# Performance work log

Measured on AMD Instinct MI355X. Metric: run time of the kernel, lower is better.

Reference implementation:

```python
import jax, jax.numpy as jnp
import numpy as np

SIZE = 896
HALF = SIZE // 2
BINS = 256  # 2 ** (16 / 2)


def _scale(idx):
    # map bin index [0, BINS-1] -> [-1, 1]
    return idx.astype(jnp.float32) / ((BINS - 1) / 2.0) - 1.0


def setup_inputs() -> dict:
    key = jax.random.key(0)
    ks = jax.random.split(key, 13)
    B, T = 32, 256
    rn = lambda k, shape, s: jax.random.normal(k, shape, dtype=jnp.float32) * s
    return {
        "conditional": rn(ks[0], (B, T, 3, SIZE), 0.1),
        "hidden_state": rn(ks[1], (B, SIZE), 0.1),
        "gru_input_bias": rn(ks[2], (3 * SIZE,), 0.1),
        "gru_hidden_weight": rn(ks[3], (3 * SIZE, SIZE), 0.05),
        "gru_hidden_bias": rn(ks[4], (3 * SIZE,), 0.1),
        "w_coarse_in": rn(ks[5], (3 * HALF, 2), 0.5),
        "b_coarse_in": rn(ks[6], (3 * HALF,), 0.1),
        "w_fine_in": rn(ks[7], (3 * HALF, 3), 0.5),
        "b_fine_in": rn(ks[8], (3 * HALF,), 0.1),
        "w_bins_coarse": rn(ks[9], (BINS, HALF), 0.05),
        "b_bins_coarse": rn(ks[10], (BINS,), 0.1),
        "w_bins_fine": rn(ks[11], (BINS, HALF), 0.05),
        "b_bins_fine": rn(ks[12], (BINS,), 0.1),
    }


def reference(conditional, hidden_state, gru_input_bias, gru_hidden_weight,
              gru_hidden_bias, w_coarse_in, b_coarse_in, w_fine_in, b_fine_in,
              w_bins_coarse, b_bins_coarse, w_bins_fine, b_bins_fine):
    B = conditional.shape[0]
    # add GRU input biases per gate (r, u, e)
    cond = conditional + gru_input_bias.reshape(3, SIZE)  # [B,T,3,SIZE]
    # split each gate into coarse/fine halves and regroup: [B,T,3*HALF]
    cond_c = jnp.concatenate([cond[:, :, 0, :HALF], cond[:, :, 1, :HALF], cond[:, :, 2, :HALF]], axis=-1)
    cond_f = jnp.concatenate([cond[:, :, 0, HALF:], cond[:, :, 1, HALF:], cond[:, :, 2, HALF:]], axis=-1)
    cond_c = jnp.swapaxes(cond_c, 0, 1)  # [T,B,3*HALF] time-major for scan
    cond_f = jnp.swapaxes(cond_f, 0, 1)

    # initial go-sample: split_signal(0) -> coarse bin 128, fine bin 0
    coarse0 = jnp.full((B, 1), 128.0 / 127.5 - 1.0, dtype=jnp.float32)
    fine0 = jnp.full((B, 1), -1.0, dtype=jnp.float32)
    ch0 = hidden_state[:, :HALF]
    fh0 = hidden_state[:, HALF:]

    def step(carry, x):
        coarse, fine, ch, fh = carry
        xc, xf = x
        hp = jnp.concatenate([ch, fh], axis=1) @ gru_hidden_weight.T + gru_hidden_bias  # [B,3*SIZE]
        hcr, hfr, hcu, hfu, hce, hfe = jnp.split(hp, 6, axis=1)  # each [B,HALF]
        # ---- coarse half-GRU ----
        ci = jnp.concatenate([coarse, fine], axis=1)  # [B,2]
        cp = ci @ w_coarse_in.T + b_coarse_in + xc  # [B,3*HALF]
        ru = jax.nn.sigmoid(cp[:, :SIZE] + jnp.concatenate([hcr, hcu], axis=1))
        r, u = ru[:, :HALF], ru[:, HALF:]
        e = jnp.tanh(r * hce + cp[:, SIZE:])
        ch = u * ch + (1.0 - u) * e
        c_idx = jnp.argmax(ch @ w_bins_coarse.T + b_bins_coarse, axis=1)  # [B]
        coarse = _scale(c_idx)[:, None]
        # ---- fine half-GRU ----
        fi = jnp.concatenate([ci, coarse], axis=1)  # [B,3]
        fp = fi @ w_fine_in.T + b_fine_in + xf
        ru = jax.nn.sigmoid(fp[:, :SIZE] + jnp.concatenate([hfr, hfu], axis=1))
        r, u = ru[:, :HALF], ru[:, HALF:]
        e = jnp.tanh(r * hfe + fp[:, SIZE:])
        fh = u * fh + (1.0 - u) * e
        f_idx = jnp.argmax(fh @ w_bins_fine.T + b_bins_fine, axis=1)
        fine = _scale(f_idx)[:, None]
        return (coarse, fine, ch, fh), (c_idx, f_idx)

    (_, _, ch, fh), (oc, of) = jax.lax.scan(step, (coarse0, fine0, ch0, fh0), (cond_c, cond_f))
    hidden = jnp.concatenate([ch, fh], axis=1)  # [B,SIZE]
    return jnp.swapaxes(oc, 0, 1), jnp.swapaxes(of, 0, 1), hidden
```

## Files before the change

### kernel.cpp

```cpp
#include <hip/hip_runtime.h>

#define NWG  56
#define NBLK 57
#define NTHR 384
#define TT   256
#define SPLITF   2048.0f
#define INVSPLIT 4.8828125e-4f

typedef _Float16 f16;
typedef __attribute__((ext_vector_type(8))) _Float16 f16x8;
typedef __attribute__((ext_vector_type(4))) float f32x4;

__device__ __forceinline__ float sigacc(float x){ return 1.0f/(1.0f + expf(-x)); }

__device__ __forceinline__ unsigned long long amax_key(float v, int bin, unsigned tag){
  unsigned u = __float_as_uint(v);
  u = (u & 0x80000000u) ? ~u : (u | 0x80000000u);
  return ((unsigned long long)u << 32) | ((unsigned long long)(tag & 0xFFFFu) << 8)
       | (unsigned)(255 - bin);
}

__device__ __forceinline__ int grp_base(int g){ return 448 * ((g < 3) ? (2*g) : (2*g - 5)); }

__device__ __forceinline__ void xchg32(unsigned* p, unsigned v){
  __hip_atomic_exchange(p, v, __ATOMIC_RELAXED, __HIP_MEMORY_SCOPE_AGENT);
}
__device__ __forceinline__ void xchg64(unsigned long long* p, unsigned long long v){
  __hip_atomic_exchange(p, v, __ATOMIC_RELAXED, __HIP_MEMORY_SCOPE_AGENT);
}
__device__ __forceinline__ unsigned ldg32(const unsigned* p){
  return __hip_atomic_load(p, __ATOMIC_RELAXED, __HIP_MEMORY_SCOPE_AGENT);
}
__device__ __forceinline__ unsigned long long ldg64(const void* p){
  return __hip_atomic_load((const unsigned long long*)p, __ATOMIC_RELAXED, __HIP_MEMORY_SCOPE_AGENT);
}
__device__ __forceinline__ void drain(){ asm volatile("s_waitcnt vmcnt(0)" ::: "memory"); }
__device__ __forceinline__ int f16bits(f16 h){
  return (int)__builtin_bit_cast(unsigned short, h);
}

__global__ void pack_gru(const float* __restrict__ W, f16* __restrict__ outH, f16* __restrict__ outL){
  int blk = blockIdx.x;
  int ks  = blk % 14;
  int rest= blk / 14;
  int wv  = rest % 6, w = rest / 6;
  int mt  = wv >> 1, kh = wv & 1;
  int l   = threadIdx.x;
  int lr  = mt*16 + (l & 15);
  int R   = grp_base(lr >> 3) + 8*w + (lr & 7);
  int k   = kh*448 + ks*32 + (l >> 4)*8;
  const float* src = W + (size_t)R*896 + k;
  f16x8 vh, vl;
  #pragma unroll
  for (int i=0;i<8;i++){
    float x = src[i];
    f16 h = (f16)x;
    vh[i] = h;
    vl[i] = (f16)((x - (float)h) * SPLITF);
  }
  size_t o = (size_t)blk*64 + l;
  ((f16x8*)outH)[o] = vh;
  ((f16x8*)outL)[o] = vl;
}

__global__ void pack_bins(const float* __restrict__ Wc, const float* __restrict__ Wf,
                          f16* __restrict__ oCh, f16* __restrict__ oCl,
                          f16* __restrict__ oFh, f16* __restrict__ oFl){
  int blk  = blockIdx.x;
  int half = blk / 224;
  int rem  = blk % 224;
  int ks   = rem % 14, wg = rem / 14;
  int l    = threadIdx.x;
  const float* W = half ? Wf : Wc;
  f16* oh = half ? oFh : oCh;
  f16* ol = half ? oFl : oCl;
  int bin = wg*16 + (l & 15);
  int k   = ks*32 + (l >> 4)*8;
  const float* src = W + (size_t)bin*448 + k;
  f16x8 vh, vl;
  #pragma unroll
  for (int i=0;i<8;i++){
    float x = src[i];
    f16 h = (f16)x;
    vh[i] = h;
    vl[i] = (f16)((x - (float)h) * SPLITF);
  }
  size_t o = (size_t)rem*64 + l;
  ((f16x8*)oh)[o] = vh;
  ((f16x8*)ol)[o] = vl;
}

__launch_bounds__(NTHR, 1)
__global__ void wavernn_main(
    const float* __restrict__ cond,
    const float* __restrict__ h0,
    const float* __restrict__ gib,
    const float* __restrict__ ghb,
    const float* __restrict__ wci,
    const float* __restrict__ bci,
    const float* __restrict__ wfi,
    const float* __restrict__ bfi,
    const float* __restrict__ bbc,
    const float* __restrict__ bbf,
    const f16*  __restrict__ wsAh, const f16* __restrict__ wsAl,
    const f16*  __restrict__ wsBCh, const f16* __restrict__ wsBCl,
    const f16*  __restrict__ wsBFh, const f16* __restrict__ wsBFl,
    unsigned*   __restrict__ Hg,
    unsigned long long* __restrict__ partC,
    unsigned long long* __restrict__ partF,
    unsigned*   __restrict__ flags,
    unsigned*   __restrict__ resC,
    unsigned*   __restrict__ resF,
    float* __restrict__ out)
{
  __shared__ float hpL[48][33];
  __shared__ float coarseL[32], fineL[32];
  __shared__ f16x8 binBh0[896], binBl0[896], binBh1[896], binBl1[896];
  __shared__ float wclL[3][8][2], bclL[3][8], wflL[3][8][3], bflL[3][8], hblL[48];

  const int w   = blockIdx.x;
  const int tid = threadIdx.x;
  const int wv  = tid >> 6;
  const int l   = tid & 63;

  auto poll_parts = [&](const unsigned long long* part, unsigned tgt)->unsigned long long {
    int bb = l & 31;
    unsigned long long k0,k1,k2,k3,k4,k5,k6,k7,k8,k9,k10,k11,k12,k13,k14,k15;
    for(;;){
      k0=ldg64(&part[0*32+bb]);  k1=ldg64(&part[1*32+bb]);
      k2=ldg64(&part[2*32+bb]);  k3=ldg64(&part[3*32+bb]);
      k4=ldg64(&part[4*32+bb]);  k5=ldg64(&part[5*32+bb]);
      k6=ldg64(&part[6*32+bb]);  k7=ldg64(&part[7*32+bb]);
      k8=ldg64(&part[8*32+bb]);  k9=ldg64(&part[9*32+bb]);
      k10=ldg64(&part[10*32+bb]); k11=ldg64(&part[11*32+bb]);
      k12=ldg64(&part[12*32+bb]); k13=ldg64(&part[13*32+bb]);
      k14=ldg64(&part[14*32+bb]); k15=ldg64(&part[15*32+bb]);
      unsigned long long tmask = 0xFFFF00ull, texp = (unsigned long long)tgt << 8;
      bool ok = ((k0&tmask)==texp) & ((k1&tmask)==texp) & ((k2&tmask)==texp) & ((k3&tmask)==texp)
              & ((k4&tmask)==texp) & ((k5&tmask)==texp) & ((k6&tmask)==texp) & ((k7&tmask)==texp)
              & ((k8&tmask)==texp) & ((k9&tmask)==texp) & ((k10&tmask)==texp)& ((k11&tmask)==texp)
              & ((k12&tmask)==texp)& ((k13&tmask)==texp)& ((k14&tmask)==texp)& ((k15&tmask)==texp);
      if (__all(ok)) break;
      __builtin_amdgcn_s_sleep(1);
    }
    unsigned long long m01=k0>k1?k0:k1, m23=k2>k3?k2:k3, m45=k4>k5?k4:k5, m67=k6>k7?k6:k7;
    unsigned long long m89=k8>k9?k8:k9, mab=k10>k11?k10:k11, mcd=k12>k13?k12:k13, mef=k14>k15?k14:k15;
    unsigned long long a=m01>m23?m01:m23, c2=m45>m67?m45:m67, d=m89>mab?m89:mab, f=mcd>mef?mcd:mef;
    unsigned long long x=a>c2?a:c2, y=d>f?d:f;
    return x>y?x:y;
  };

  if (w == NWG) {
    if (wv == 0) {
      for (int t=0; t<TT; t++){
        unsigned tgt = (unsigned)(t+1);
        unsigned long long best = poll_parts(partC, tgt);
        int bin = 255 - (int)(best & 0xFFull);
        if (l < 32) {
          out[l*TT + t] = (float)bin;
          xchg32(&resC[l], (tgt << 16) | (unsigned)bin);
        }
      }
    } else if (wv == 1) {
      for (int t=0; t<TT; t++){
        unsigned tgt = (unsigned)(t+1);
        unsigned long long best = poll_parts(partF, tgt);
        int bin = 255 - (int)(best & 0xFFull);
        if (l < 32) {
          out[8192 + l*TT + t] = (float)bin;
          xchg32(&resF[l], (tgt << 16) | (unsigned)bin);
        }
      }
    }
    return;
  }

  const int b   = tid >> 3, e = tid & 7;
  const bool owner = tid < 256;
  const int jc  = 8*w + e;

  unsigned* fE0 = flags;
  unsigned* fE1 = flags + 64;
  unsigned* fE3 = flags + 128;

  const int g_kh = (wv >= 2 && wv <= 4) ? 0 : 1;
  const int g_mt = (wv >= 2 && wv <= 4) ? (wv - 2) : (wv == 5 ? 2 : wv);

  f16x8 afh[14], afl[14];
  {
    const f16x8* Ah = (const f16x8*)wsAh + (size_t)(w*6 + (g_mt*2 + g_kh))*14*64;
    const f16x8* Al = (const f16x8*)wsAl + (size_t)(w*6 + (g_mt*2 + g_kh))*14*64;
    #pragma unroll
    for (int ks=0; ks<14; ks++){ afh[ks] = Ah[ks*64 + l]; afl[ks] = Al[ks*64 + l]; }
  }
  if (w < 16) {
    const f16x8* s0 = (const f16x8*)wsBCh + (size_t)w*896;
    const f16x8* s1 = (const f16x8*)wsBCl + (size_t)w*896;
    const f16x8* s2 = (const f16x8*)wsBFh + (size_t)w*896;
    const f16x8* s3 = (const f16x8*)wsBFl + (size_t)w*896;
    for (int i = tid; i < 896; i += NTHR) {
      binBh0[i] = s0[i]; binBl0[i] = s1[i];
      binBh1[i] = s2[i]; binBl1[i] = s3[i];
    }
  }
  if (tid < 48) hblL[tid] = ghb[grp_base(tid>>3) + 8*w + (tid&7)];
  if (tid < 24) {
    int p = tid >> 3, ee = tid & 7;
    int j = p*448 + 8*w + ee;
    wclL[p][ee][0] = wci[j*2+0]; wclL[p][ee][1] = wci[j*2+1];
    bclL[p][ee]    = bci[j] + gib[p*896 + 8*w + ee];
    wflL[p][ee][0] = wfi[j*3+0]; wflL[p][ee][1] = wfi[j*3+1]; wflL[p][ee][2] = wfi[j*3+2];
    bflL[p][ee]    = bfi[j] + gib[p*896 + 448 + 8*w + ee];
  }
  if (tid < 32) { coarseL[tid] = 128.0f/127.5f - 1.0f; fineL[tid] = -1.0f; }
  float biasC = 0.f, biasF = 0.f;
  if (w < 16) { biasC = bbc[w*16 + (l&15)]; biasF = bbf[w*16 + (l&15)]; }

  auto store_half = [&](unsigned* Hrow, int fine, float val){
    f16 hh = (f16)val;
    f16 hl = (f16)((val - (float)hh) * SPLITF);
    int pk = f16bits(hh) | (f16bits(hl) << 16);
    int nb = __shfl_down(pk, 1);
    if (!(e & 1)) {
      int off = fine*224 + (jc >> 1);
      unsigned hi32 = (unsigned)((pk & 0xffff) | (nb << 16));
      unsigned lo32 = ((unsigned)pk >> 16) | ((unsigned)nb & 0xffff0000u);
      xchg32(Hrow + off,       hi32);
      xchg32(Hrow + 448 + off, lo32);
    }
  };

  auto wait56 = [&](const unsigned* f, int n, unsigned tgt){
    const unsigned* p = f + ((l < n) ? l : 0);
    for(;;){
      unsigned v = ldg32(p);
      if (__all(v == tgt)) break;
      __builtin_amdgcn_s_sleep(1);
    }
    unsigned vv = __hip_atomic_load(p, __ATOMIC_ACQUIRE, __HIP_MEMORY_SCOPE_AGENT);
    asm volatile("" :: "v"(vv) : "memory");
  };
  auto poll_res = [&](const unsigned* res, unsigned tgt)->int{
    const unsigned* p = res + (l & 31);
    unsigned v;
    for(;;){
      v = ldg32(p);
      if (__all((v >> 16) == tgt)) break;
      __builtin_amdgcn_s_sleep(1);
    }
    asm volatile("" ::: "memory");
    return (int)(v & 0xFFFFu);
  };

  float chS = 0.f, fhS = 0.f;
  if (owner) {
    chS = h0[b*896 + jc];
    fhS = h0[b*896 + 448 + jc];
    unsigned* Hrow = Hg + b*896;
    store_half(Hrow, 0, chS);
    store_half(Hrow, 1, fhS);
  }
  drain();
  __syncthreads();
  if (tid == 0) xchg32(&fE0[w], 1u);
  if (wv == 0) wait56(fE0, 56, 1u);
  __syncthreads();

  float xcr=0, xcu=0, xce=0, xfr=0, xfu=0, xfe=0;
  auto prefetch = [&](int t){
    if (owner) {
      const float* cb_ = cond + ((size_t)b*TT + t)*2688;
      xcr = cb_[jc];        xcu = cb_[896 + jc];  xce = cb_[1792 + jc];
      xfr = cb_[448 + jc];  xfu = cb_[1344 + jc]; xfe = cb_[2240 + jc];
    }
  };
  auto gemm_half = [&](const unsigned* H, bool add){
    f32x4 ah0={0,0,0,0}, al0={0,0,0,0}, ah1={0,0,0,0}, al1={0,0,0,0};
    const f16* base0 = (const f16*)(H + (size_t)(l&15)*896 + g_kh*224 + (l>>4)*4);
    const f16* base1 = (const f16*)(H + (size_t)((l&15)+16)*896 + g_kh*224 + (l>>4)*4);
    #pragma unroll
    for (int ks=0; ks<14; ks++) {
      f16x8 bh0 = *(const f16x8*)(base0 + ks*32);
      f16x8 bl0 = *(const f16x8*)(base0 + 896 + ks*32);
      f16x8 bh1 = *(const f16x8*)(base1 + ks*32);
      f16x8 bl1 = *(const f16x8*)(base1 + 896 + ks*32);
      ah0 = __builtin_amdgcn_mfma_f32_16x16x32_f16(afh[ks], bh0, ah0, 0,0,0);
      al0 = __builtin_amdgcn_mfma_f32_16x16x32_f16(afh[ks], bl0, al0, 0,0,0);
      al0 = __builtin_amdgcn_mfma_f32_16x16x32_f16(afl[ks], bh0, al0, 0,0,0);
      ah1 = __builtin_amdgcn_mfma_f32_16x16x32_f16(afh[ks], bh1, ah1, 0,0,0);
      al1 = __builtin_amdgcn_mfma_f32_16x16x32_f16(afh[ks], bl1, al1, 0,0,0);
      al1 = __builtin_amdgcn_mfma_f32_16x16x32_f16(afl[ks], bh1, al1, 0,0,0);
    }
    #pragma unroll
    for (int i=0;i<4;i++){
      int row = g_mt*16 + (l>>4)*4 + i;
      float v0 = ah0[i] + al0[i]*INVSPLIT;
      float v1 = ah1[i] + al1[i]*INVSPLIT;
      if (!add) {
        hpL[row][l&15]      = v0 + hblL[row];
        hpL[row][16+(l&15)] = v1 + hblL[row];
      } else {
        hpL[row][l&15]      += v0;
        hpL[row][16+(l&15)] += v1;
      }
    }
  };
  auto do_bins = [&](const unsigned* H, int fine, const f16x8* Bh, const f16x8* Bl,
                     float bias, unsigned long long* part, unsigned tgt, int ntb){
    f32x4 acch={0,0,0,0}, accl={0,0,0,0};
    const f16* ar = (const f16*)(H + (size_t)(ntb*16 + (l&15))*896 + fine*224 + (l>>4)*4);
    #pragma unroll
    for (int ks=0; ks<14; ks++) {
      f16x8 ah  = *(const f16x8*)(ar + ks*32);
      f16x8 al_ = *(const f16x8*)(ar + 896 + ks*32);
      f16x8 bh = Bh[ks*64 + l];
      f16x8 bl = Bl[ks*64 + l];
      acch = __builtin_amdgcn_mfma_f32_16x16x32_f16(ah,  bh, acch, 0,0,0);
      accl = __builtin_amdgcn_mfma_f32_16x16x32_f16(ah,  bl, accl, 0,0,0);
      accl = __builtin_amdgcn_mfma_f32_16x16x32_f16(al_, bh, accl, 0,0,0);
    }
    #pragma unroll
    for (int i=0;i<4;i++){
      unsigned long long key = amax_key(acch[i] + accl[i]*INVSPLIT + bias, w*16 + (l&15), tgt);
      #pragma unroll
      for (int m=1; m<16; m<<=1){
        unsigned long long o = __shfl_xor(key, m, 16);
        key = (o > key) ? o : key;
      }
      if ((l&15)==0) xchg64(&part[w*32 + ntb*16 + (l>>4)*4 + i], key);
    }
  };

  prefetch(0);
  if (g_kh == 0) gemm_half(Hg, false);
  __syncthreads();
  if (g_kh == 1) gemm_half(Hg, true);
  __syncthreads();

  for (int t=0; t<TT; t++) {
    unsigned* Hn = Hg + (((t+1)&1) ? 28672 : 0);
    const unsigned tgt = (unsigned)(t+1);

    float cprev = 0.f, fprev = 0.f, hfr_ = 0.f, hfu_ = 0.f, hfe_ = 0.f;
    if (owner) {
      cprev = coarseL[b]; fprev = fineL[b];
      float cpr = cprev*wclL[0][e][0] + fprev*wclL[0][e][1] + bclL[0][e] + xcr;
      float cpu_= cprev*wclL[1][e][0] + fprev*wclL[1][e][1] + bclL[1][e] + xcu;
      float cpe = cprev*wclL[2][e][0] + fprev*wclL[2][e][1] + bclL[2][e] + xce;
      float r  = sigacc(cpr  + hpL[e][b]);
      float u  = sigacc(cpu_ + hpL[8+e][b]);
      float g  = tanhf(fmaf(r, hpL[16+e][b], cpe));
      hfr_ = hpL[24+e][b]; hfu_ = hpL[32+e][b]; hfe_ = hpL[40+e][b];
      chS = fmaf(u, chS - g, g);
      store_half(Hn + b*896, 0, chS);
    }
    drain();
    __syncthreads();
    if (tid == 0) xchg32(&fE1[w], tgt);
    if (wv == 0) wait56(fE1, 56, tgt);
    __syncthreads();

    if (w < 16 && wv < 2) do_bins(Hn, 0, binBh0, binBl0, biasC, partC, tgt, wv);
    if (g_kh == 0) gemm_half(Hn, false);
    if (wv == 5) {
      int bin = poll_res(resC, tgt);
      if (l < 32) coarseL[l] = (float)bin * (1.0f/127.5f) - 1.0f;
    }
    __syncthreads();

    if (owner) {
      float cnew = coarseL[b];
      float fpr = cprev*wflL[0][e][0] + fprev*wflL[0][e][1] + cnew*wflL[0][e][2] + bflL[0][e] + xfr;
      float fpu = cprev*wflL[1][e][0] + fprev*wflL[1][e][1] + cnew*wflL[1][e][2] + bflL[1][e] + xfu;
      float fpe = cprev*wflL[2][e][0] + fprev*wflL[2][e][1] + cnew*wflL[2][e][2] + bflL[2][e] + xfe;
      float r  = sigacc(fpr + hfr_);
      float u  = sigacc(fpu + hfu_);
      float g  = tanhf(fmaf(r, hfe_, fpe));
      fhS = fmaf(u, fhS - g, g);
      store_half(Hn + b*896, 1, fhS);
    }
    drain();
    __syncthreads();
    if (tid == 0) xchg32(&fE3[w], tgt);
    if (t < TT-1) prefetch(t+1);
    if (wv == 0) wait56(fE3, 56, tgt);
    __syncthreads();

    if (w < 16 && (wv == 2 || wv == 3)) do_bins(Hn, 1, binBh1, binBl1, biasF, partF, tgt, wv-2);
    if (g_kh == 1) gemm_half(Hn, true);
    if (wv == 4) {
      int bin = poll_res(resF, tgt);
      if (l < 32) fineL[l] = (float)bin * (1.0f/127.5f) - 1.0f;
    }
    __syncthreads();
  }

  if (owner) {
    out[16384 + b*896 + jc]        = chS;
    out[16384 + b*896 + 448 + jc]  = fhS;
  }
}

#define WS_AH    0u
#define WS_AL    4816896u
#define WS_BCH   9633792u
#define WS_BCL   9863168u
#define WS_BFH   10092544u
#define WS_BFL   10321920u
#define WS_HG    10551296u
#define WS_FLAGS 10780672u
#define WS_PC    10781696u
#define WS_PF    10785792u
#define WS_RES   10789888u

extern "C" void kernel_launch(void* const* d_in, const int* in_sizes, int n_in,
                              void* d_out, int out_size, void* d_ws, size_t ws_size,
                              hipStream_t stream) {
  const float* conditional = (const float*)d_in[0];
  const float* hidden0     = (const float*)d_in[1];
  const float* gib         = (const float*)d_in[2];
  const float* ghw         = (const float*)d_in[3];
  const float* ghb         = (const float*)d_in[4];
  const float* wci         = (const float*)d_in[5];
  const float* bci         = (const float*)d_in[6];
  const float* wfi         = (const float*)d_in[7];
  const float* bfi         = (const float*)d_in[8];
  const float* wbc         = (const float*)d_in[9];
  const float* bbc         = (const float*)d_in[10];
  const float* wbf         = (const float*)d_in[11];
  const float* bbf         = (const float*)d_in[12];

  char* ws = (char*)d_ws;
  f16* wsAh  = (f16*)(ws + WS_AH);
  f16* wsAl  = (f16*)(ws + WS_AL);
  f16* wsBCh = (f16*)(ws + WS_BCH);
  f16* wsBCl = (f16*)(ws + WS_BCL);
  f16* wsBFh = (f16*)(ws + WS_BFH);
  f16* wsBFl = (f16*)(ws + WS_BFL);
  unsigned* Hg = (unsigned*)(ws + WS_HG);
  unsigned* flags = (unsigned*)(ws + WS_FLAGS);
  unsigned long long* partC = (unsigned long long*)(ws + WS_PC);
  unsigned long long* partF = (unsigned long long*)(ws + WS_PF);
  unsigned* resC = (unsigned*)(ws + WS_RES);
  unsigned* resF = (unsigned*)(ws + WS_RES + 128);
  float* out = (float*)d_out;

  hipMemsetAsync(ws + WS_FLAGS, 0, 16384, stream);
  pack_gru<<<dim3(56*6*14), dim3(64), 0, stream>>>(ghw, wsAh, wsAl);
  pack_bins<<<dim3(448), dim3(64), 0, stream>>>(wbc, wbf, wsBCh, wsBCl, wsBFh, wsBFl);
  wavernn_main<<<dim3(NBLK), dim3(NTHR), 0, stream>>>(
      conditional, hidden0, gib, ghb, wci, bci, wfi, bfi, bbc, bbf,
      wsAh, wsAl, wsBCh, wsBCl, wsBFh, wsBFl,
      Hg, partC, partF, flags, resC, resF, out);
}
```

Baseline: 5.903 ms.

## Pad sync flags to cache lines and chunk hidden-state exchange layout

Spreads the per-workgroup flags and result slots to 64-byte strides so that different writers no longer share cache lines. It also changes the global hidden-state exchange buffer into per-(batch, workgroup) 64-byte chunks, with each writer emitting two 64-bit stores instead of several 32-bit ones. The GEMM and bin readers are re-indexed to match. The aim is to cut false sharing and store traffic on the latency-bound cross-workgroup sync path, at the cost of more scattered reads by consumers.

```diff
diff --git a/kernel.cpp b/kernel.cpp
--- a/kernel.cpp
+++ b/kernel.cpp
@@ -158,7 +158,7 @@
         int bin = 255 - (int)(best & 0xFFull);
         if (l < 32) {
           out[l*TT + t] = (float)bin;
-          xchg32(&resC[l], (tgt << 16) | (unsigned)bin);
+          xchg32(&resC[l*16], (tgt << 16) | (unsigned)bin);
         }
       }
     } else if (wv == 1) {
@@ -168,7 +168,7 @@
         int bin = 255 - (int)(best & 0xFFull);
         if (l < 32) {
           out[8192 + l*TT + t] = (float)bin;
-          xchg32(&resF[l], (tgt << 16) | (unsigned)bin);
+          xchg32(&resF[l*16], (tgt << 16) | (unsigned)bin);
         }
       }
     }
@@ -180,8 +180,8 @@
   const int jc  = 8*w + e;
 
   unsigned* fE0 = flags;
-  unsigned* fE1 = flags + 64;
-  unsigned* fE3 = flags + 128;
+  unsigned* fE1 = flags + 1024;
+  unsigned* fE3 = flags + 2048;
 
   const int g_kh = (wv >= 2 && wv <= 4) ? 0 : 1;
   const int g_mt = (wv >= 2 && wv <= 4) ? (wv - 2) : (wv == 5 ? 2 : wv);
@@ -216,22 +216,28 @@
   float biasC = 0.f, biasF = 0.f;
   if (w < 16) { biasC = bbc[w*16 + (l&15)]; biasF = bbf[w*16 + (l&15)]; }
 
-  auto store_half = [&](unsigned* Hrow, int fine, float val){
+  auto store_half = [&](unsigned* Hc, int fine, float val){
     f16 hh = (f16)val;
     f16 hl = (f16)((val - (float)hh) * SPLITF);
     int pk = f16bits(hh) | (f16bits(hl) << 16);
-    int nb = __shfl_down(pk, 1);
-    if (!(e & 1)) {
-      int off = fine*224 + (jc >> 1);
-      unsigned hi32 = (unsigned)((pk & 0xffff) | (nb << 16));
-      unsigned lo32 = ((unsigned)pk >> 16) | ((unsigned)nb & 0xffff0000u);
-      xchg32(Hrow + off,       hi32);
-      xchg32(Hrow + 448 + off, lo32);
+    int n1 = __shfl_down(pk, 1);
+    int n2 = __shfl_down(pk, 2);
+    int n3 = __shfl_down(pk, 3);
+    if ((e & 3) == 0) {
+      unsigned h0_ = (unsigned)((pk & 0xffff) | (n1 << 16));
+      unsigned h1_ = (unsigned)((n2 & 0xffff) | (n3 << 16));
+      unsigned l0_ = ((unsigned)pk >> 16) | ((unsigned)n1 & 0xffff0000u);
+      unsigned l1_ = ((unsigned)n2 >> 16) | ((unsigned)n3 & 0xffff0000u);
+      int q = e >> 2;
+      xchg64((unsigned long long*)(Hc + fine*8 + q*2),
+             (unsigned long long)h0_ | ((unsigned long long)h1_ << 32));
+      xchg64((unsigned long long*)(Hc + fine*8 + 4 + q*2),
+             (unsigned long long)l0_ | ((unsigned long long)l1_ << 32));
     }
   };
 
   auto wait56 = [&](const unsigned* f, int n, unsigned tgt){
-    const unsigned* p = f + ((l < n) ? l : 0);
+    const unsigned* p = f + ((l < n) ? l*16 : 0);
     for(;;){
       unsigned v = ldg32(p);
       if (__all(v == tgt)) break;
@@ -241,7 +247,7 @@
     asm volatile("" :: "v"(vv) : "memory");
   };
   auto poll_res = [&](const unsigned* res, unsigned tgt)->int{
-    const unsigned* p = res + (l & 31);
+    const unsigned* p = res + (l & 31)*16;
     unsigned v;
     for(;;){
       v = ldg32(p);
@@ -256,13 +262,13 @@
   if (owner) {
     chS = h0[b*896 + jc];
     fhS = h0[b*896 + 448 + jc];
-    unsigned* Hrow = Hg + b*896;
-    store_half(Hrow, 0, chS);
-    store_half(Hrow, 1, fhS);
+    unsigned* Hc = Hg + (b*56 + w)*16;
+    store_half(Hc, 0, chS);
+    store_half(Hc, 1, fhS);
   }
   drain();
   __syncthreads();
-  if (tid == 0) xchg32(&fE0[w], 1u);
+  if (tid == 0) xchg32(&fE0[w*16], 1u);
   if (wv == 0) wait56(fE0, 56, 1u);
   __syncthreads();
 
@@ -276,14 +282,16 @@
   };
   auto gemm_half = [&](const unsigned* H, bool add){
     f32x4 ah0={0,0,0,0}, al0={0,0,0,0}, ah1={0,0,0,0}, al1={0,0,0,0};
-    const f16* base0 = (const f16*)(H + (size_t)(l&15)*896 + g_kh*224 + (l>>4)*4);
-    const f16* base1 = (const f16*)(H + (size_t)((l&15)+16)*896 + g_kh*224 + (l>>4)*4);
+    const unsigned* c0 = H + ((size_t)(l&15)*56 + (l>>4))*16 + g_kh*8;
+    const unsigned* c1 = c0 + 16*56*16;
     #pragma unroll
     for (int ks=0; ks<14; ks++) {
-      f16x8 bh0 = *(const f16x8*)(base0 + ks*32);
-      f16x8 bl0 = *(const f16x8*)(base0 + 896 + ks*32);
-      f16x8 bh1 = *(const f16x8*)(base1 + ks*32);
-      f16x8 bl1 = *(const f16x8*)(base1 + 896 + ks*32);
+      const unsigned* p0 = c0 + ks*64;
+      const unsigned* p1 = c1 + ks*64;
+      f16x8 bh0 = *(const f16x8*)(p0);
+      f16x8 bl0 = *(const f16x8*)(p0 + 4);
+      f16x8 bh1 = *(const f16x8*)(p1);
+      f16x8 bl1 = *(const f16x8*)(p1 + 4);
       ah0 = __builtin_amdgcn_mfma_f32_16x16x32_f16(afh[ks], bh0, ah0, 0,0,0);
       al0 = __builtin_amdgcn_mfma_f32_16x16x32_f16(afh[ks], bl0, al0, 0,0,0);
       al0 = __builtin_amdgcn_mfma_f32_16x16x32_f16(afl[ks], bh0, al0, 0,0,0);
@@ -308,11 +316,12 @@
   auto do_bins = [&](const unsigned* H, int fine, const f16x8* Bh, const f16x8* Bl,
                      float bias, unsigned long long* part, unsigned tgt, int ntb){
     f32x4 acch={0,0,0,0}, accl={0,0,0,0};
-    const f16* ar = (const f16*)(H + (size_t)(ntb*16 + (l&15))*896 + fine*224 + (l>>4)*4);
+    const unsigned* ar = H + ((size_t)(ntb*16 + (l&15))*56 + (l>>4))*16 + fine*8;
     #pragma unroll
     for (int ks=0; ks<14; ks++) {
-      f16x8 ah  = *(const f16x8*)(ar + ks*32);
-      f16x8 al_ = *(const f16x8*)(ar + 896 + ks*32);
+      const unsigned* p = ar + ks*64;
+      f16x8 ah  = *(const f16x8*)(p);
+      f16x8 al_ = *(const f16x8*)(p + 4);
       f16x8 bh = Bh[ks*64 + l];
       f16x8 bl = Bl[ks*64 + l];
       acch = __builtin_amdgcn_mfma_f32_16x16x32_f16(ah,  bh, acch, 0,0,0);
@@ -352,11 +361,11 @@
       float g  = tanhf(fmaf(r, hpL[16+e][b], cpe));
       hfr_ = hpL[24+e][b]; hfu_ = hpL[32+e][b]; hfe_ = hpL[40+e][b];
       chS = fmaf(u, chS - g, g);
-      store_half(Hn + b*896, 0, chS);
+      store_half(Hn + (b*56 + w)*16, 0, chS);
     }
     drain();
     __syncthreads();
-    if (tid == 0) xchg32(&fE1[w], tgt);
+    if (tid == 0) xchg32(&fE1[w*16], tgt);
     if (wv == 0) wait56(fE1, 56, tgt);
     __syncthreads();
 
@@ -377,11 +386,11 @@
       float u  = sigacc(fpu + hfu_);
       float g  = tanhf(fmaf(r, hfe_, fpe));
       fhS = fmaf(u, fhS - g, g);
-      store_half(Hn + b*896, 1, fhS);
+      store_half(Hn + (b*56 + w)*16, 1, fhS);
     }
     drain();
     __syncthreads();
-    if (tid == 0) xchg32(&fE3[w], tgt);
+    if (tid == 0) xchg32(&fE3[w*16], tgt);
     if (t < TT-1) prefetch(t+1);
     if (wv == 0) wait56(fE3, 56, tgt);
     __syncthreads();
@@ -409,9 +418,9 @@
 #define WS_BFL   10321920u
 #define WS_HG    10551296u
 #define WS_FLAGS 10780672u
-#define WS_PC    10781696u
-#define WS_PF    10785792u
-#define WS_RES   10789888u
+#define WS_RES   10792960u
+#define WS_PC    10797056u
+#define WS_PF    10801152u
 
 extern "C" void kernel_launch(void* const* d_in, const int* in_sizes, int n_in,
                               void* d_out, int out_size, void* d_ws, size_t ws_size,
@@ -439,13 +448,13 @@
   f16* wsBFl = (f16*)(ws + WS_BFL);
   unsigned* Hg = (unsigned*)(ws + WS_HG);
   unsigned* flags = (unsigned*)(ws + WS_FLAGS);
+  unsigned* resC = (unsigned*)(ws + WS_RES);
+  unsigned* resF = (unsigned*)(ws + WS_RES + 2048);
   unsigned long long* partC = (unsigned long long*)(ws + WS_PC);
   unsigned long long* partF = (unsigned long long*)(ws + WS_PF);
-  unsigned* resC = (unsigned*)(ws + WS_RES);
-  unsigned* resF = (unsigned*)(ws + WS_RES + 128);
   float* out = (float*)d_out;
 
-  hipMemsetAsync(ws + WS_FLAGS, 0, 16384, stream);
+  hipMemsetAsync(ws + WS_FLAGS, 0, 24576, stream);
   pack_gru<<<dim3(56*6*14), dim3(64), 0, stream>>>(ghw, wsAh, wsAl);
   pack_bins<<<dim3(448), dim3(64), 0, stream>>>(wbc, wbf, wsBCh, wsBCl, wsBFh, wsBFl);
   wavernn_main<<<dim3(NBLK), dim3(NTHR), 0, stream>>>(
```

Result: faster. 5.578 ms (-5.5%).
